# Kernel optimization log

Measured on AMD Instinct MI355X. Metric: run time of the kernel, lower is better.

The kernel has to match this reference:

```python
import jax, jax.numpy as jnp
import numpy as np

TEMP = 100000.0  # extreme temperature -> softmax ~ hard argmax of nearest past keyframe


def setup_inputs() -> dict:
    key = jax.random.key(0)
    k1, k2, k3 = jax.random.split(key, 3)
    B, T_in, N, T_out = 16, 64, 52, 4096
    root_positions = jax.random.normal(k1, (B, T_in, 3), dtype=jnp.float32)
    joint_rotations_ortho6d = jax.random.normal(k2, (B, T_in, N, 6), dtype=jnp.float32)
    input_frame_indices = jnp.sort(jax.random.randint(k3, (T_in,), 0, T_out, dtype=jnp.int64))
    # guarantee a past keyframe exists for every target (avoids all -inf column / NaN)
    input_frame_indices = input_frame_indices.at[0].set(0)
    target_frame_indices = jnp.arange(T_out, dtype=jnp.int64)
    return {
        "root_positions": root_positions,
        "joint_rotations_ortho6d": joint_rotations_ortho6d,
        "input_frame_indices": input_frame_indices,
        "target_frame_indices": target_frame_indices,
    }


def _zero_velocity(root_positions, joint_rotations_ortho6d,
                   input_frame_indices, target_frame_indices, nb_joints):
    # [T_in, T_out] timestamp differences; future keyframes (diff > 0) masked out
    diff = (input_frame_indices[:, None] - target_frame_indices[None, :]).astype(jnp.float32)
    diff = jnp.where(diff > 0.0, -jnp.inf, diff)
    diff = diff - jnp.max(diff, axis=0, keepdims=True)
    weights = jax.nn.softmax(TEMP * diff, axis=0)  # [T_in, T_out], ~one-hot per column

    # root position: [B, T_in, 3] x [T_in, T_out] -> [B, T_out, 3]
    root = jnp.einsum('btc,ts->bsc', root_positions, weights)
    B, T_out = root.shape[0], root.shape[1]
    # repeat across joints -> [B, T_out, N, 3]
    joint_positions = jnp.broadcast_to(root[:, :, None, :], (B, T_out, nb_joints, 3))
    joint_positions = jnp.asarray(joint_positions)

    # rotations: [B, T_in, N, 6] x [T_in, T_out] -> [B, T_out, N, 6]
    joint_rotations = jnp.einsum('btnc,ts->bsnc', joint_rotations_ortho6d, weights)
    return joint_positions, joint_rotations


def _pad_time(x, t_in):
    # prepend first frame repeated (t_in - 1) times, append last frame once
    front = jnp.repeat(x[:, :1], t_in - 1, axis=1)
    return jnp.concatenate([front, x, x[:, -1:]], axis=1)


def reference(root_positions, joint_rotations_ortho6d,
              input_frame_indices, target_frame_indices):
    nb_joints = joint_rotations_ortho6d.shape[2]
    jp, jr = _zero_velocity(root_positions, joint_rotations_ortho6d,
                            input_frame_indices, target_frame_indices, nb_joints)
    t_in = input_frame_indices.shape[0]
    return _pad_time(jp, t_in), _pad_time(jr, t_in)
```

## Files before the change

### kernel.cpp

```cpp
#include <hip/hip_runtime.h>

constexpr int B     = 16;
constexpr int T_IN  = 64;
constexpr int NJ    = 52;
constexpr int T_OUT = 4096;
constexpr int T_PAD = T_OUT + T_IN;

constexpr int JP_ROW4 = NJ * 3 / 4;
constexpr int JR_ROW4 = NJ * 6 / 4;
constexpr int NROWS   = B * T_PAD;
constexpr int NP4     = NROWS * JP_ROW4;

constexpr int CHUNK  = 32;
constexpr int NCHUNK = T_PAD / CHUNK;

typedef float f4 __attribute__((ext_vector_type(4)));

__global__ __launch_bounds__(256) void zv_run(
    const float* __restrict__ root,
    const float* __restrict__ rot,
    const int*   __restrict__ idx,
    f4*          __restrict__ out4)
{
    __shared__ int   sidx[T_IN];
    __shared__ int   ssel[CHUNK];
    __shared__ float sinv[CHUNK];
    __shared__ f4    srm[CHUNK];

    const int tid = threadIdx.x;
    const int cs  = blockIdx.x * CHUNK;
    const int b   = blockIdx.y;

    if (tid < T_IN) sidx[tid] = idx[tid];
    __syncthreads();

    if (tid < CHUNK) {
        const int s_out = cs + tid;
        int s = s_out - (T_IN - 1);
        s = s < 0 ? 0 : (s > T_OUT - 1 ? T_OUT - 1 : s);
        int ub = 0;
        #pragma unroll
        for (int st = 64; st > 0; st >>= 1)
            if (ub + st <= T_IN && sidx[ub + st - 1] <= s) ub += st;
        const int m = sidx[ub - 1];
        int lo = 0;
        #pragma unroll
        for (int st = 32; st > 0; st >>= 1)
            if (sidx[lo + st - 1] < m) lo += st;
        const int   k   = ub - lo;
        const float inv = 1.0f / (float)k;
        ssel[tid] = lo | (k << 8);
        sinv[tid] = inv;
        const float* rp = root + (size_t)(b * T_IN + lo) * 3;
        float r0 = rp[0], r1 = rp[1], r2 = rp[2];
        for (int q = 1; q < k; ++q) { r0 += rp[3*q]; r1 += rp[3*q+1]; r2 += rp[3*q+2]; }
        f4 v; v.x = r0 * inv; v.y = r1 * inv; v.z = r2 * inv; v.w = 0.f;
        srm[tid] = v;
    }
    __syncthreads();

    {
        f4* dst = out4 + (size_t)(b * T_PAD + cs) * JP_ROW4;
        for (int u = tid; u < CHUNK * JP_ROW4; u += 256) {
            const int r  = u / JP_ROW4;
            const int md = u % 3;
            const f4  rm = srm[r];
            f4 v;
            v.x = md == 0 ? rm.x : (md == 1 ? rm.y : rm.z);
            v.y = md == 0 ? rm.y : (md == 1 ? rm.z : rm.x);
            v.z = md == 0 ? rm.z : (md == 1 ? rm.x : rm.y);
            v.w = v.x;
            dst[u] = v;
        }
    }

    if (tid < 234) {
        const int e = tid % 78;
        const int j = tid / 78;
        const f4* rotb = (const f4*)rot + ((size_t)b * T_IN * JR_ROW4 + e);
        f4*       dst  = out4 + (NP4 + (size_t)(b * T_PAD + cs) * JR_ROW4 + e);
        int cur = -1;
        f4  a;
        for (int r = j; r < CHUNK; r += 3) {
            const int selr = ssel[r];
            if (selr != cur) {
                cur = selr;
                const int lo = cur & 0xff;
                const int k  = cur >> 8;
                const f4* src = rotb + (size_t)lo * JR_ROW4;
                a = src[0];
                for (int q = 1; q < k; ++q) a += src[(size_t)q * JR_ROW4];
                a *= sinv[r];
            }
            dst[(size_t)r * JR_ROW4] = a;
        }
    }
}

extern "C" void kernel_launch(void* const* d_in, const int* in_sizes, int n_in,
                              void* d_out, int out_size, void* d_ws, size_t ws_size,
                              hipStream_t stream) {
    const float* root = (const float*)d_in[0];
    const float* rot  = (const float*)d_in[1];
    const int*   idx  = (const int*)d_in[2];
    f4* out4 = (f4*)d_out;

    hipLaunchKernelGGL(zv_run, dim3(NCHUNK, B), dim3(256), 0, stream,
                       root, rot, idx, out4);
}
```

Measured before the change: 26.96 us.

## Split position and rotation writes into separate blocks with larger time segments

Blocks are now specialized: half of the grid writes rotation outputs and half writes the broadcast root positions, each over 160-frame segments instead of 32. Root values are prebuilt in shared memory as three rotated f4 patterns so the position writer just copies without per-element selects. Rotation threads find runs of identical keyframe selection and write the averaged value repeatedly without reloading. This cuts the block count, per-block search overhead and redundant loads, but grid parallelism drops (26x32 blocks) and work per block is less balanced.

```diff
diff --git a/kernel.cpp b/kernel.cpp
--- a/kernel.cpp
+++ b/kernel.cpp
@@ -9,33 +9,34 @@
 constexpr int JP_ROW4 = NJ * 3 / 4;
 constexpr int JR_ROW4 = NJ * 6 / 4;
 constexpr int NROWS   = B * T_PAD;
-constexpr int NP4     = NROWS * JP_ROW4;
+constexpr size_t NP4  = (size_t)NROWS * JP_ROW4;
 
-constexpr int CHUNK  = 32;
-constexpr int NCHUNK = T_PAD / CHUNK;
+constexpr int SEG  = 160;
+constexpr int NSEG = T_PAD / SEG;
 
 typedef float f4 __attribute__((ext_vector_type(4)));
 
-__global__ __launch_bounds__(256) void zv_run(
+__global__ __launch_bounds__(256) void zv_burst(
     const float* __restrict__ root,
     const float* __restrict__ rot,
     const int*   __restrict__ idx,
     f4*          __restrict__ out4)
 {
     __shared__ int   sidx[T_IN];
-    __shared__ int   ssel[CHUNK];
-    __shared__ float sinv[CHUNK];
-    __shared__ f4    srm[CHUNK];
+    __shared__ int   ssel[SEG];
+    __shared__ float sinv[SEG];
+    __shared__ f4    spat[SEG * 3];
 
-    const int tid = threadIdx.x;
-    const int cs  = blockIdx.x * CHUNK;
-    const int b   = blockIdx.y;
+    const int  tid   = threadIdx.x;
+    const int  seg0  = blockIdx.x * SEG;
+    const bool is_jr = blockIdx.y < B;
+    const int  b     = is_jr ? blockIdx.y : blockIdx.y - B;
 
     if (tid < T_IN) sidx[tid] = idx[tid];
     __syncthreads();
 
-    if (tid < CHUNK) {
-        const int s_out = cs + tid;
+    if (tid < SEG) {
+        const int s_out = seg0 + tid;
         int s = s_out - (T_IN - 1);
         s = s < 0 ? 0 : (s > T_OUT - 1 ? T_OUT - 1 : s);
         int ub = 0;
@@ -49,50 +50,60 @@
             if (sidx[lo + st - 1] < m) lo += st;
         const int   k   = ub - lo;
         const float inv = 1.0f / (float)k;
-        ssel[tid] = lo | (k << 8);
-        sinv[tid] = inv;
-        const float* rp = root + (size_t)(b * T_IN + lo) * 3;
-        float r0 = rp[0], r1 = rp[1], r2 = rp[2];
-        for (int q = 1; q < k; ++q) { r0 += rp[3*q]; r1 += rp[3*q+1]; r2 += rp[3*q+2]; }
-        f4 v; v.x = r0 * inv; v.y = r1 * inv; v.z = r2 * inv; v.w = 0.f;
-        srm[tid] = v;
+        if (is_jr) {
+            ssel[tid] = lo | (k << 8);
+            sinv[tid] = inv;
+        } else {
+            const float* rp = root + (size_t)(b * T_IN + lo) * 3;
+            float r0 = rp[0], r1 = rp[1], r2 = rp[2];
+            for (int q = 1; q < k; ++q) { r0 += rp[3*q]; r1 += rp[3*q+1]; r2 += rp[3*q+2]; }
+            r0 *= inv; r1 *= inv; r2 *= inv;
+            f4 v0; v0.x = r0; v0.y = r1; v0.z = r2; v0.w = r0;
+            f4 v1; v1.x = r1; v1.y = r2; v1.z = r0; v1.w = r1;
+            f4 v2; v2.x = r2; v2.y = r0; v2.z = r1; v2.w = r2;
+            spat[tid * 3 + 0] = v0;
+            spat[tid * 3 + 1] = v1;
+            spat[tid * 3 + 2] = v2;
+        }
     }
     __syncthreads();
 
-    {
-        f4* dst = out4 + (size_t)(b * T_PAD + cs) * JP_ROW4;
-        for (int u = tid; u < CHUNK * JP_ROW4; u += 256) {
-            const int r  = u / JP_ROW4;
-            const int md = u % 3;
-            const f4  rm = srm[r];
-            f4 v;
-            v.x = md == 0 ? rm.x : (md == 1 ? rm.y : rm.z);
-            v.y = md == 0 ? rm.y : (md == 1 ? rm.z : rm.x);
-            v.z = md == 0 ? rm.z : (md == 1 ? rm.x : rm.y);
-            v.w = v.x;
-            dst[u] = v;
-        }
-    }
+    if (tid >= 234) return;
 
-    if (tid < 234) {
+    if (is_jr) {
         const int e = tid % 78;
         const int j = tid / 78;
         const f4* rotb = (const f4*)rot + ((size_t)b * T_IN * JR_ROW4 + e);
-        f4*       dst  = out4 + (NP4 + (size_t)(b * T_PAD + cs) * JR_ROW4 + e);
-        int cur = -1;
-        f4  a;
-        for (int r = j; r < CHUNK; r += 3) {
-            const int selr = ssel[r];
-            if (selr != cur) {
-                cur = selr;
-                const int lo = cur & 0xff;
-                const int k  = cur >> 8;
-                const f4* src = rotb + (size_t)lo * JR_ROW4;
-                a = src[0];
+        f4*       dst  = out4 + (NP4 + (size_t)(b * T_PAD + seg0) * JR_ROW4 + e);
+        int r = j;
+        while (r < SEG) {
+            const int sel = ssel[r];
+            const int lo  = sel & 0xff;
+            const int k   = sel >> 8;
+            const f4* src = rotb + (size_t)lo * JR_ROW4;
+            f4 a = src[0];
+            if (k > 1) {
                 for (int q = 1; q < k; ++q) a += src[(size_t)q * JR_ROW4];
                 a *= sinv[r];
             }
-            dst[(size_t)r * JR_ROW4] = a;
+            int re = r;
+            while (re + 3 < SEG && ssel[re + 3] == sel) re += 3;
+            for (int q = r; q <= re; q += 3)
+                dst[(size_t)q * JR_ROW4] = a;
+            r = re + 3;
+        }
+    } else {
+        const int p  = tid % 39;
+        const int r0 = tid / 39;
+        const int md = p % 3;
+        f4* dst = out4 + ((size_t)(b * T_PAD + seg0) * JP_ROW4 + tid);
+        int pi = r0 * 3 + md;
+        #pragma unroll 4
+        for (int it = 0; it < SEG / 6; ++it) {
+            dst[(size_t)it * 234] = spat[pi + it * 18];
+        }
+        if (r0 < 4) {
+            dst[(size_t)(SEG / 6) * 234] = spat[pi + (SEG / 6) * 18];
         }
     }
 }
@@ -105,6 +116,6 @@
     const int*   idx  = (const int*)d_in[2];
     f4* out4 = (f4*)d_out;
 
-    hipLaunchKernelGGL(zv_run, dim3(NCHUNK, B), dim3(256), 0, stream,
+    hipLaunchKernelGGL(zv_burst, dim3(NSEG, 2 * B), dim3(256), 0, stream,
                        root, rot, idx, out4);
 }
```

Result: slower. 30.90 us (+14.6%).
